# Kernel tuning notes

Hardware: AMD Instinct MI355X
Metric: run time of the kernel (lower is better)

The kernel has to match this reference:

```python
import jax, jax.numpy as jnp
import numpy as np

B, T, S, H, L = 64, 512, 400, 768, 9


def setup_inputs() -> dict:
    rng = np.random.default_rng(0)
    attn = np.zeros((B, T), np.int32)
    ids_lens = np.zeros((B, S), np.int32)
    for bi in range(B):
        Lb = int(rng.integers(T // 2, T + 1))  # valid wordpiece count
        lens = []
        rem = Lb
        while rem > 0 and len(lens) < S - 1:
            l = int(min(rng.integers(1, 4), rem))  # 1-3 wordpieces per word
            lens.append(l)
            rem -= l
        if rem > 0:
            lens.append(rem)
        attn[bi, :Lb] = 1
        ids_lens[bi, :len(lens)] = np.asarray(lens, np.int32)
    label_ids = rng.integers(0, L, (B, S)).astype(np.int32)
    label_mask = ids_lens > 0
    key = jax.random.key(0)
    k1, k2 = jax.random.split(key)
    last_enc_out = jax.random.normal(k1, (B, T, H), jnp.float32)
    W = jax.random.normal(k2, (H, L), jnp.float32) * 0.02
    b = jnp.zeros((L,), jnp.float32)
    return {
        'last_enc_out': last_enc_out, 'W': W, 'b': b,
        'attention_mask': jnp.asarray(attn), 'ids_lens': jnp.asarray(ids_lens),
        'label_ids': jnp.asarray(label_ids), 'label_mask': jnp.asarray(label_mask),
    }


def reference(last_enc_out, W, b, attention_mask, ids_lens, label_ids, label_mask):
    Bv, Tv, Hv = last_enc_out.shape
    Sv = ids_lens.shape[1]
    # position of each valid token among the row's valid tokens
    tok_pos = jnp.cumsum(attention_mask, axis=1) - 1            # [B,T]
    cum = jnp.cumsum(ids_lens, axis=1)                          # [B,S] nondecreasing
    # word index for each token: first w with cum[w] > tok_pos
    word_idx = jax.vmap(lambda c, p: jnp.searchsorted(c, p, side='right'))(cum, tok_pos)
    valid = attention_mask > 0
    seg = jnp.where(valid, jnp.arange(Bv)[:, None] * Sv + word_idx, Bv * Sv)  # dump slot for pad
    sums = jax.ops.segment_sum(last_enc_out.reshape(Bv * Tv, Hv), seg.reshape(Bv * Tv),
                               num_segments=Bv * Sv + 1)[:Bv * Sv]
    counts = jnp.maximum(ids_lens.reshape(Bv * Sv), 1).astype(last_enc_out.dtype)
    means = (sums / counts[:, None]).reshape(Bv, Sv, Hv)
    word_mask = ids_lens > 0
    bert_embed = jnp.where(word_mask[:, :, None], means, jnp.zeros((), last_enc_out.dtype))
    # dropout is identity in eval mode
    logits = bert_embed @ W + b                                 # [B,S,L]
    logp = jax.nn.log_softmax(logits, axis=-1)
    nll = -jnp.take_along_axis(logp, label_ids[..., None].astype(jnp.int32), axis=-1)[..., 0]
    mf = label_mask.astype(logits.dtype)
    loss = jnp.sum(nll * mf) / jnp.sum(mf)                      # CE with ignore_index masking
    output = jnp.argmax(logits, axis=-1)
    return loss, output
```

## Files before the change

kernel.cpp:

```cpp
#include <hip/hip_runtime.h>
#include <math.h>

#define Bdim 64
#define Tdim 512
#define Sdim 400
#define Hdim 768
#define Ldim 9
#define PSTRIDE 12

#define PROJ_BLOCKS 2048
#define ROWS_PER_BLK 16

template <int CTRL>
__device__ __forceinline__ float dpp_add(float x) {
  int y = __builtin_amdgcn_update_dpp(0, __float_as_int(x), CTRL, 0xF, 0xF, false);
  return x + __int_as_float(y);
}
__device__ __forceinline__ float wave_sum63(float x) {
  x = dpp_add<0x111>(x);
  x = dpp_add<0x112>(x);
  x = dpp_add<0x114>(x);
  x = dpp_add<0x118>(x);
  x = dpp_add<0x142>(x);
  x = dpp_add<0x143>(x);
  return x;
}

__global__ __launch_bounds__(192, 4) void proj_kernel(
    const float* __restrict__ enc, const float* __restrict__ W,
    float* __restrict__ proj, float* __restrict__ accum,
    unsigned* __restrict__ counter) {
  int tid = threadIdx.x;
  int lane = tid & 63;
  int w = tid >> 6;
  int l0 = w * 3;
  int base = blockIdx.x * ROWS_PER_BLK;

  if (blockIdx.x == 0) {
    if (tid < 2) accum[tid] = 0.0f;
    if (tid == 2) *counter = 0u;
  }

  float wf[3][4][3];
#pragma unroll
  for (int k = 0; k < 3; ++k)
#pragma unroll
    for (int j = 0; j < 4; ++j) {
      int h = 4 * lane + 256 * k + j;
#pragma unroll
      for (int c = 0; c < 3; ++c) wf[k][j][c] = W[(size_t)h * Ldim + l0 + c];
    }

  const float4* encf4 = (const float4*)enc;

  float4 xa0, xa1, xa2, xb0, xb1, xb2;
#define LDROW(v0, v1, v2, IDX)                                             \
  {                                                                        \
    const float4* r_ = encf4 + (size_t)(base + (IDX)) * (Hdim / 4);        \
    v0 = r_[lane]; v1 = r_[lane + 64]; v2 = r_[lane + 128];                \
  }
#define PROCROW(v0, v1, v2, IDX)                                           \
  {                                                                        \
    float dd[3];                                                           \
    _Pragma("unroll") for (int c = 0; c < 3; ++c) {                        \
      dd[c] = v0.x * wf[0][0][c] + v0.y * wf[0][1][c] +                    \
              v0.z * wf[0][2][c] + v0.w * wf[0][3][c] +                    \
              v1.x * wf[1][0][c] + v1.y * wf[1][1][c] +                    \
              v1.z * wf[1][2][c] + v1.w * wf[1][3][c] +                    \
              v2.x * wf[2][0][c] + v2.y * wf[2][1][c] +                    \
              v2.z * wf[2][2][c] + v2.w * wf[2][3][c];                     \
      dd[c] = wave_sum63(dd[c]);                                           \
    }                                                                      \
    if (lane == 63) {                                                      \
      float* dst = proj + (size_t)(base + (IDX)) * PSTRIDE + l0;           \
      dst[0] = dd[0]; dst[1] = dd[1]; dst[2] = dd[2];                      \
    }                                                                      \
  }

  LDROW(xa0, xa1, xa2, 0)
  LDROW(xb0, xb1, xb2, 1)
#pragma unroll
  for (int i = 0; i < ROWS_PER_BLK; i += 2) {
    PROCROW(xa0, xa1, xa2, i)
    if (i + 2 < ROWS_PER_BLK) LDROW(xa0, xa1, xa2, i + 2)
    PROCROW(xb0, xb1, xb2, i + 1)
    if (i + 3 < ROWS_PER_BLK) LDROW(xb0, xb1, xb2, i + 3)
  }
#undef LDROW
#undef PROCROW
}

__global__ __launch_bounds__(Tdim) void rowword_kernel(
    const float* __restrict__ proj, const float* __restrict__ bias,
    const int* __restrict__ attn, const int* __restrict__ ids_lens,
    const int* __restrict__ label_ids, float* __restrict__ out,
    float* __restrict__ accum, unsigned* __restrict__ counter) {
  int b = blockIdx.x;
  int tid = threadIdx.x;
  int lane = tid & 63, wid = tid >> 6;
  __shared__ int p2t[Tdim];
  __shared__ int wst[Sdim];
  __shared__ int wsum[8];
  __shared__ int totsm;
  __shared__ float ssm[8], csm[8];

  int m = attn[b * Tdim + tid];
  int x = m;
#pragma unroll
  for (int off = 1; off < 64; off <<= 1) {
    int v = __shfl_up(x, off, 64);
    if (lane >= off) x += v;
  }
  if (lane == 63) wsum[wid] = x;
  __syncthreads();
  if (tid < 8) {
    int s = wsum[tid], y = s;
#pragma unroll
    for (int off = 1; off < 8; off <<= 1) {
      int v = __shfl_up(y, off, 64);
      if (tid >= off) y += v;
    }
    wsum[tid] = y - s;
    if (tid == 7) totsm = y;
  }
  __syncthreads();
  x += wsum[wid];
  if (m) p2t[x - 1] = tid;
  int nv_local = totsm;
  __syncthreads();

  int len = (tid < Sdim) ? ids_lens[b * Sdim + tid] : 0;
  int x2 = len;
#pragma unroll
  for (int off = 1; off < 64; off <<= 1) {
    int v = __shfl_up(x2, off, 64);
    if (lane >= off) x2 += v;
  }
  if (lane == 63) wsum[wid] = x2;
  __syncthreads();
  if (tid < 8) {
    int s = wsum[tid], y = s;
#pragma unroll
    for (int off = 1; off < 8; off <<= 1) {
      int v = __shfl_up(y, off, 64);
      if (tid >= off) y += v;
    }
    wsum[tid] = y - s;
  }
  __syncthreads();
  x2 += wsum[wid];
  if (tid < Sdim) wst[tid] = x2 - len;
  __syncthreads();

  float nll = 0.0f, cnt = 0.0f;
  if (tid < Sdim) {
    int bs = b * Sdim + tid;
    float sum[Ldim];
#pragma unroll
    for (int l = 0; l < Ldim; ++l) sum[l] = 0.0f;
    if (len > 0) {
      int start = wst[tid];
      for (int j = 0; j < len; ++j) {
        int q = start + j;
        if (q >= nv_local) break;
        const float* pr = proj + ((size_t)(b << 9) + p2t[q]) * PSTRIDE;
        const float4* pr4 = (const float4*)pr;
        float4 r0 = pr4[0], r1 = pr4[1];
        float r8 = pr[8];
        sum[0] += r0.x; sum[1] += r0.y; sum[2] += r0.z; sum[3] += r0.w;
        sum[4] += r1.x; sum[5] += r1.y; sum[6] += r1.z; sum[7] += r1.w;
        sum[8] += r8;
      }
    }
    float inv = (len > 0) ? 1.0f / (float)len : 0.0f;
    float lg[Ldim];
#pragma unroll
    for (int l = 0; l < Ldim; ++l) lg[l] = sum[l] * inv + bias[l];

    int amax = 0;
    float mx = lg[0];
#pragma unroll
    for (int l = 1; l < Ldim; ++l)
      if (lg[l] > mx) { mx = lg[l]; amax = l; }
    out[1 + bs] = (float)amax;

    if (len > 0) {
      float se = 0.0f;
#pragma unroll
      for (int l = 0; l < Ldim; ++l) se += expf(lg[l] - mx);
      float lse = mx + logf(se);
      int lab = label_ids[bs];
      float ll = lg[0];
#pragma unroll
      for (int l = 1; l < Ldim; ++l) ll = (lab == l) ? lg[l] : ll;
      nll = lse - ll;
      cnt = 1.0f;
    }
  }

#pragma unroll
  for (int off = 32; off > 0; off >>= 1) {
    nll += __shfl_down(nll, off, 64);
    cnt += __shfl_down(cnt, off, 64);
  }
  if (lane == 0) { ssm[wid] = nll; csm[wid] = cnt; }
  __syncthreads();
  if (tid == 0) {
    float S = 0.f, C = 0.f;
#pragma unroll
    for (int k = 0; k < 8; ++k) { S += ssm[k]; C += csm[k]; }
    atomicAdd(&accum[0], S);
    atomicAdd(&accum[1], C);
    __threadfence();
    unsigned prev = atomicAdd(counter, 1u);
    if (prev == gridDim.x - 1) {
      __threadfence();
      float Sf = atomicAdd(&accum[0], 0.0f);
      float Cf = atomicAdd(&accum[1], 0.0f);
      out[0] = Sf / Cf;
    }
  }
}

extern "C" void kernel_launch(void* const* d_in, const int* in_sizes, int n_in,
                              void* d_out, int out_size, void* d_ws, size_t ws_size,
                              hipStream_t stream) {
  const float* enc     = (const float*)d_in[0];
  const float* W       = (const float*)d_in[1];
  const float* bias    = (const float*)d_in[2];
  const int* attn      = (const int*)d_in[3];
  const int* ids_lens  = (const int*)d_in[4];
  const int* label_ids = (const int*)d_in[5];

  float* out = (float*)d_out;

  char* ws = (char*)d_ws;
  size_t off0 = 0;
  float* accum      = (float*)(ws + off0);    off0 += 128;
  unsigned* counter = (unsigned*)(ws + off0); off0 += 128;
  float* proj       = (float*)(ws + off0);    off0 += (size_t)Bdim * Tdim * PSTRIDE * sizeof(float);

  proj_kernel<<<PROJ_BLOCKS, 192, 0, stream>>>(enc, W, proj, accum, counter);
  rowword_kernel<<<Bdim, Tdim, 0, stream>>>(proj, bias, attn, ids_lens,
                                            label_ids, out, accum, counter);
}
```

Measured before the change: 34.58 us.

## Skip padded token rows in projection and split word pass across four blocks per row

```diff
diff --git a/kernel.cpp b/kernel.cpp
--- a/kernel.cpp
+++ b/kernel.cpp
@@ -26,10 +26,10 @@
   return x;
 }
 
-__global__ __launch_bounds__(192, 4) void proj_kernel(
+__global__ __launch_bounds__(192) void proj_kernel(
     const float* __restrict__ enc, const float* __restrict__ W,
-    float* __restrict__ proj, float* __restrict__ accum,
-    unsigned* __restrict__ counter) {
+    const int* __restrict__ attn, float* __restrict__ proj,
+    float* __restrict__ accum, unsigned* __restrict__ counter) {
   int tid = threadIdx.x;
   int lane = tid & 63;
   int w = tid >> 6;
@@ -41,6 +41,11 @@
     if (tid == 2) *counter = 0u;
   }
 
+  int mybit = attn[base + (lane & 15)];
+  unsigned long long bal = __ballot(mybit != 0);
+  unsigned mask = (unsigned)(bal & 0xFFFFu);
+  if (mask == 0) return;
+
   float wf[3][4][3];
 #pragma unroll
   for (int k = 0; k < 3; ++k)
@@ -54,13 +59,14 @@
   const float4* encf4 = (const float4*)enc;
 
   float4 xa0, xa1, xa2, xb0, xb1, xb2;
+#define VALID(I) ((I) < ROWS_PER_BLK && (mask >> (I)) & 1u)
 #define LDROW(v0, v1, v2, IDX)                                             \
-  {                                                                        \
+  if (VALID(IDX)) {                                                        \
     const float4* r_ = encf4 + (size_t)(base + (IDX)) * (Hdim / 4);        \
     v0 = r_[lane]; v1 = r_[lane + 64]; v2 = r_[lane + 128];                \
   }
 #define PROCROW(v0, v1, v2, IDX)                                           \
-  {                                                                        \
+  if (VALID(IDX)) {                                                        \
     float dd[3];                                                           \
     _Pragma("unroll") for (int c = 0; c < 3; ++c) {                        \
       dd[c] = v0.x * wf[0][0][c] + v0.y * wf[0][1][c] +                    \
@@ -82,10 +88,11 @@
 #pragma unroll
   for (int i = 0; i < ROWS_PER_BLK; i += 2) {
     PROCROW(xa0, xa1, xa2, i)
-    if (i + 2 < ROWS_PER_BLK) LDROW(xa0, xa1, xa2, i + 2)
+    LDROW(xa0, xa1, xa2, i + 2)
     PROCROW(xb0, xb1, xb2, i + 1)
-    if (i + 3 < ROWS_PER_BLK) LDROW(xb0, xb1, xb2, i + 3)
-  }
+    LDROW(xb0, xb1, xb2, i + 3)
+  }
+#undef VALID
 #undef LDROW
 #undef PROCROW
 }
@@ -95,7 +102,8 @@
     const int* __restrict__ attn, const int* __restrict__ ids_lens,
     const int* __restrict__ label_ids, float* __restrict__ out,
     float* __restrict__ accum, unsigned* __restrict__ counter) {
-  int b = blockIdx.x;
+  int b = blockIdx.x >> 2;
+  int part = blockIdx.x & 3;
   int tid = threadIdx.x;
   int lane = tid & 63, wid = tid >> 6;
   __shared__ int p2t[Tdim];
@@ -153,14 +161,16 @@
   __syncthreads();
 
   float nll = 0.0f, cnt = 0.0f;
-  if (tid < Sdim) {
-    int bs = b * Sdim + tid;
+  int s_word = part * 100 + tid;
+  if (tid < 100) {
+    int bs = b * Sdim + s_word;
+    int wlen = ids_lens[bs];
     float sum[Ldim];
 #pragma unroll
     for (int l = 0; l < Ldim; ++l) sum[l] = 0.0f;
-    if (len > 0) {
-      int start = wst[tid];
-      for (int j = 0; j < len; ++j) {
+    if (wlen > 0) {
+      int start = wst[s_word];
+      for (int j = 0; j < wlen; ++j) {
         int q = start + j;
         if (q >= nv_local) break;
         const float* pr = proj + ((size_t)(b << 9) + p2t[q]) * PSTRIDE;
@@ -172,7 +182,7 @@
         sum[8] += r8;
       }
     }
-    float inv = (len > 0) ? 1.0f / (float)len : 0.0f;
+    float inv = (wlen > 0) ? 1.0f / (float)wlen : 0.0f;
     float lg[Ldim];
 #pragma unroll
     for (int l = 0; l < Ldim; ++l) lg[l] = sum[l] * inv + bias[l];
@@ -184,7 +194,7 @@
       if (lg[l] > mx) { mx = lg[l]; amax = l; }
     out[1 + bs] = (float)amax;
 
-    if (len > 0) {
+    if (wlen > 0) {
       float se = 0.0f;
 #pragma unroll
       for (int l = 0; l < Ldim; ++l) se += expf(lg[l] - mx);
@@ -240,7 +250,7 @@
   unsigned* counter = (unsigned*)(ws + off0); off0 += 128;
   float* proj       = (float*)(ws + off0);    off0 += (size_t)Bdim * Tdim * PSTRIDE * sizeof(float);
 
-  proj_kernel<<<PROJ_BLOCKS, 192, 0, stream>>>(enc, W, proj, accum, counter);
-  rowword_kernel<<<Bdim, Tdim, 0, stream>>>(proj, bias, attn, ids_lens,
-                                            label_ids, out, accum, counter);
-}
+  proj_kernel<<<PROJ_BLOCKS, 192, 0, stream>>>(enc, W, attn, proj, accum, counter);
+  rowword_kernel<<<Bdim * 4, Tdim, 0, stream>>>(proj, bias, attn, ids_lens,
+                                                label_ids, out, accum, counter);
+}
```

Result: slower. 39.48 us (+14.2%).

## Split hidden dim across waves in projection and reduce partials via LDS

Applied to the files above, without the earlier changes.

```diff
diff --git a/kernel.cpp b/kernel.cpp
--- a/kernel.cpp
+++ b/kernel.cpp
@@ -33,7 +33,6 @@
   int tid = threadIdx.x;
   int lane = tid & 63;
   int w = tid >> 6;
-  int l0 = w * 3;
   int base = blockIdx.x * ROWS_PER_BLK;
 
   if (blockIdx.x == 0) {
@@ -41,53 +40,62 @@
     if (tid == 2) *counter = 0u;
   }
 
-  float wf[3][4][3];
-#pragma unroll
-  for (int k = 0; k < 3; ++k)
-#pragma unroll
-    for (int j = 0; j < 4; ++j) {
-      int h = 4 * lane + 256 * k + j;
-#pragma unroll
-      for (int c = 0; c < 3; ++c) wf[k][j][c] = W[(size_t)h * Ldim + l0 + c];
-    }
+  __shared__ float part[ROWS_PER_BLK][3][PSTRIDE];
+
+  float wf[4][Ldim];
+#pragma unroll
+  for (int j = 0; j < 4; ++j) {
+    int h = w * 256 + 4 * lane + j;
+#pragma unroll
+    for (int c = 0; c < Ldim; ++c) wf[j][c] = W[(size_t)h * Ldim + c];
+  }
 
   const float4* encf4 = (const float4*)enc;
-
-  float4 xa0, xa1, xa2, xb0, xb1, xb2;
-#define LDROW(v0, v1, v2, IDX)                                             \
+  const float4* src = encf4 + (size_t)base * (Hdim / 4) + w * 64 + lane;
+
+  float4 buf0, buf1, buf2, buf3;
+#define LDR(BUF, I) BUF = src[(size_t)(I) * (Hdim / 4)];
+#define PRC(BUF, I)                                                        \
   {                                                                        \
-    const float4* r_ = encf4 + (size_t)(base + (IDX)) * (Hdim / 4);        \
-    v0 = r_[lane]; v1 = r_[lane + 64]; v2 = r_[lane + 128];                \
-  }
-#define PROCROW(v0, v1, v2, IDX)                                           \
-  {                                                                        \
-    float dd[3];                                                           \
-    _Pragma("unroll") for (int c = 0; c < 3; ++c) {                        \
-      dd[c] = v0.x * wf[0][0][c] + v0.y * wf[0][1][c] +                    \
-              v0.z * wf[0][2][c] + v0.w * wf[0][3][c] +                    \
-              v1.x * wf[1][0][c] + v1.y * wf[1][1][c] +                    \
-              v1.z * wf[1][2][c] + v1.w * wf[1][3][c] +                    \
-              v2.x * wf[2][0][c] + v2.y * wf[2][1][c] +                    \
-              v2.z * wf[2][2][c] + v2.w * wf[2][3][c];                     \
+    float dd[Ldim];                                                        \
+    _Pragma("unroll") for (int c = 0; c < Ldim; ++c) {                     \
+      dd[c] = BUF.x * wf[0][c] + BUF.y * wf[1][c] +                        \
+              BUF.z * wf[2][c] + BUF.w * wf[3][c];                         \
       dd[c] = wave_sum63(dd[c]);                                           \
     }                                                                      \
     if (lane == 63) {                                                      \
-      float* dst = proj + (size_t)(base + (IDX)) * PSTRIDE + l0;           \
-      dst[0] = dd[0]; dst[1] = dd[1]; dst[2] = dd[2];                      \
+      _Pragma("unroll") for (int c = 0; c < Ldim; ++c)                     \
+        part[I][w][c] = dd[c];                                             \
     }                                                                      \
   }
 
-  LDROW(xa0, xa1, xa2, 0)
-  LDROW(xb0, xb1, xb2, 1)
-#pragma unroll
-  for (int i = 0; i < ROWS_PER_BLK; i += 2) {
-    PROCROW(xa0, xa1, xa2, i)
-    if (i + 2 < ROWS_PER_BLK) LDROW(xa0, xa1, xa2, i + 2)
-    PROCROW(xb0, xb1, xb2, i + 1)
-    if (i + 3 < ROWS_PER_BLK) LDROW(xb0, xb1, xb2, i + 3)
-  }
-#undef LDROW
-#undef PROCROW
+  LDR(buf0, 0) LDR(buf1, 1) LDR(buf2, 2) LDR(buf3, 3)
+  PRC(buf0, 0)  LDR(buf0, 4)
+  PRC(buf1, 1)  LDR(buf1, 5)
+  PRC(buf2, 2)  LDR(buf2, 6)
+  PRC(buf3, 3)  LDR(buf3, 7)
+  PRC(buf0, 4)  LDR(buf0, 8)
+  PRC(buf1, 5)  LDR(buf1, 9)
+  PRC(buf2, 6)  LDR(buf2, 10)
+  PRC(buf3, 7)  LDR(buf3, 11)
+  PRC(buf0, 8)  LDR(buf0, 12)
+  PRC(buf1, 9)  LDR(buf1, 13)
+  PRC(buf2, 10) LDR(buf2, 14)
+  PRC(buf3, 11) LDR(buf3, 15)
+  PRC(buf0, 12)
+  PRC(buf1, 13)
+  PRC(buf2, 14)
+  PRC(buf3, 15)
+#undef LDR
+#undef PRC
+
+  __syncthreads();
+  if (tid < ROWS_PER_BLK * Ldim) {
+    int row = tid / Ldim;
+    int l = tid - row * Ldim;
+    float v = part[row][0][l] + part[row][1][l] + part[row][2][l];
+    proj[(size_t)(base + row) * PSTRIDE + l] = v;
+  }
 }
 
 __global__ __launch_bounds__(Tdim) void rowword_kernel(
```

Result: slower. 40.83 us (+18.1%).

## Split wave into half-waves per row and use packed FMA in projection

Applied to the files above, without the earlier changes.

```diff
diff --git a/kernel.cpp b/kernel.cpp
--- a/kernel.cpp
+++ b/kernel.cpp
@@ -11,22 +11,23 @@
 #define PROJ_BLOCKS 2048
 #define ROWS_PER_BLK 16
 
+typedef float v2f __attribute__((ext_vector_type(2)));
+
 template <int CTRL>
 __device__ __forceinline__ float dpp_add(float x) {
   int y = __builtin_amdgcn_update_dpp(0, __float_as_int(x), CTRL, 0xF, 0xF, false);
   return x + __int_as_float(y);
 }
-__device__ __forceinline__ float wave_sum63(float x) {
+__device__ __forceinline__ float rsum32(float x) {
   x = dpp_add<0x111>(x);
   x = dpp_add<0x112>(x);
   x = dpp_add<0x114>(x);
   x = dpp_add<0x118>(x);
   x = dpp_add<0x142>(x);
-  x = dpp_add<0x143>(x);
   return x;
 }
 
-__global__ __launch_bounds__(192, 4) void proj_kernel(
+__global__ __launch_bounds__(192, 2) void proj_kernel(
     const float* __restrict__ enc, const float* __restrict__ W,
     float* __restrict__ proj, float* __restrict__ accum,
     unsigned* __restrict__ counter) {
@@ -34,6 +35,8 @@
   int lane = tid & 63;
   int w = tid >> 6;
   int l0 = w * 3;
+  int lr = lane & 31;
+  int half = lane >> 5;
   int base = blockIdx.x * ROWS_PER_BLK;
 
   if (blockIdx.x == 0) {
@@ -41,53 +44,71 @@
     if (tid == 2) *counter = 0u;
   }
 
-  float wf[3][4][3];
-#pragma unroll
-  for (int k = 0; k < 3; ++k)
-#pragma unroll
-    for (int j = 0; j < 4; ++j) {
-      int h = 4 * lane + 256 * k + j;
-#pragma unroll
-      for (int c = 0; c < 3; ++c) wf[k][j][c] = W[(size_t)h * Ldim + l0 + c];
-    }
-
-  const float4* encf4 = (const float4*)enc;
-
-  float4 xa0, xa1, xa2, xb0, xb1, xb2;
-#define LDROW(v0, v1, v2, IDX)                                             \
-  {                                                                        \
-    const float4* r_ = encf4 + (size_t)(base + (IDX)) * (Hdim / 4);        \
-    v0 = r_[lane]; v1 = r_[lane + 64]; v2 = r_[lane + 128];                \
-  }
-#define PROCROW(v0, v1, v2, IDX)                                           \
-  {                                                                        \
-    float dd[3];                                                           \
-    _Pragma("unroll") for (int c = 0; c < 3; ++c) {                        \
-      dd[c] = v0.x * wf[0][0][c] + v0.y * wf[0][1][c] +                    \
-              v0.z * wf[0][2][c] + v0.w * wf[0][3][c] +                    \
-              v1.x * wf[1][0][c] + v1.y * wf[1][1][c] +                    \
-              v1.z * wf[1][2][c] + v1.w * wf[1][3][c] +                    \
-              v2.x * wf[2][0][c] + v2.y * wf[2][1][c] +                    \
-              v2.z * wf[2][2][c] + v2.w * wf[2][3][c];                     \
-      dd[c] = wave_sum63(dd[c]);                                           \
-    }                                                                      \
-    if (lane == 63) {                                                      \
-      float* dst = proj + (size_t)(base + (IDX)) * PSTRIDE + l0;           \
-      dst[0] = dd[0]; dst[1] = dd[1]; dst[2] = dd[2];                      \
-    }                                                                      \
-  }
-
-  LDROW(xa0, xa1, xa2, 0)
-  LDROW(xb0, xb1, xb2, 1)
-#pragma unroll
-  for (int i = 0; i < ROWS_PER_BLK; i += 2) {
-    PROCROW(xa0, xa1, xa2, i)
-    if (i + 2 < ROWS_PER_BLK) LDROW(xa0, xa1, xa2, i + 2)
-    PROCROW(xb0, xb1, xb2, i + 1)
-    if (i + 3 < ROWS_PER_BLK) LDROW(xb0, xb1, xb2, i + 3)
-  }
-#undef LDROW
-#undef PROCROW
+  v2f wf[6][2][3];
+#pragma unroll
+  for (int k = 0; k < 6; ++k)
+#pragma unroll
+    for (int p = 0; p < 2; ++p)
+#pragma unroll
+      for (int c = 0; c < 3; ++c) {
+        int h = lr * 4 + k * 128 + 2 * p;
+        wf[k][p][c] = (v2f){W[(size_t)h * Ldim + l0 + c],
+                            W[(size_t)(h + 1) * Ldim + l0 + c]};
+      }
+
+  const float4* __restrict__ encf4 = (const float4*)enc;
+
+  float4 A0, A1, A2, A3, A4, A5;
+  float4 B0, B1, B2, B3, B4, B5;
+
+#define LD(S, IT)                                                             \
+  {                                                                           \
+    const float4* r_ =                                                        \
+        encf4 + (size_t)(base + 2 * (IT) + half) * (Hdim / 4) + lr;           \
+    S##0 = r_[0];   S##1 = r_[32];  S##2 = r_[64];                            \
+    S##3 = r_[96];  S##4 = r_[128]; S##5 = r_[160];                           \
+  }
+
+#define FMAK(X, K)                                                            \
+  {                                                                           \
+    v2f p0 = {X.x, X.y}, p1 = {X.z, X.w};                                     \
+    ac0 = __builtin_elementwise_fma(p0, wf[K][0][0], ac0);                    \
+    ac1 = __builtin_elementwise_fma(p0, wf[K][0][1], ac1);                    \
+    ac2 = __builtin_elementwise_fma(p0, wf[K][0][2], ac2);                    \
+    ac0 = __builtin_elementwise_fma(p1, wf[K][1][0], ac0);                    \
+    ac1 = __builtin_elementwise_fma(p1, wf[K][1][1], ac1);                    \
+    ac2 = __builtin_elementwise_fma(p1, wf[K][1][2], ac2);                    \
+  }
+
+#define STEP(S, IT, NXT)                                                      \
+  {                                                                           \
+    v2f ac0 = {0.f, 0.f}, ac1 = {0.f, 0.f}, ac2 = {0.f, 0.f};                 \
+    FMAK(S##0, 0) FMAK(S##1, 1) FMAK(S##2, 2)                                 \
+    FMAK(S##3, 3) FMAK(S##4, 4) FMAK(S##5, 5)                                 \
+    if ((NXT) < ROWS_PER_BLK / 2) LD(S, NXT)                                  \
+    float d0 = ac0.x + ac0.y;                                                 \
+    float d1 = ac1.x + ac1.y;                                                 \
+    float d2 = ac2.x + ac2.y;                                                 \
+    d0 = rsum32(d0); d1 = rsum32(d1); d2 = rsum32(d2);                        \
+    if ((lane & 31) == 31) {                                                  \
+      float* dst = proj + (size_t)(base + 2 * (IT) + half) * PSTRIDE + l0;    \
+      dst[0] = d0; dst[1] = d1; dst[2] = d2;                                  \
+    }                                                                         \
+  }
+
+  LD(A, 0)
+  LD(B, 1)
+  STEP(A, 0, 2)
+  STEP(B, 1, 3)
+  STEP(A, 2, 4)
+  STEP(B, 3, 5)
+  STEP(A, 4, 6)
+  STEP(B, 5, 7)
+  STEP(A, 6, 8)
+  STEP(B, 7, 9)
+#undef LD
+#undef FMAK
+#undef STEP
 }
 
 __global__ __launch_bounds__(Tdim) void rowword_kernel(
```

Measured after the change: 35.07 us. No clear change (+1.4%).
